# Performance work log

Hardware: AMD Instinct MI355X
Metric: run time of the kernel (lower is better)

Reference implementation:

```python
import jax, jax.numpy as jnp
import numpy as np

EPS = 1e-7  # keras.backend.epsilon()


def setup_inputs() -> dict:
    key = jax.random.key(0)
    k1, k2, k3 = jax.random.split(key, 3)
    B, N, D_in, C, D_out = 32, 2048, 8, 32, 16
    x = jax.random.normal(k1, (B, N, D_in), dtype=jnp.float32)
    W = jax.random.normal(k2, (1, N, C, D_out, D_in), dtype=jnp.float32) * 0.05
    R = jax.random.normal(k3, (1, N, C), dtype=jnp.float32)
    return {"x": x, "W": W, "R": R}


def reference(x, W, R):
    # x: [B, N, D_in]; W: [1, N, C, D_out, D_in]; R: [1, N, C]
    R_nor = jax.nn.softmax(R[0], axis=0)          # softmax over N (axis=1 of [1,N,C])
    # per-capsule transform: u[b,n,c,j] = sum_k W[n,c,j,k] * x[b,n,k]
    u = jnp.einsum('ncjk,bnk->bncj', W[0], x)
    # routing-weighted aggregation over input capsules n
    s = jnp.einsum('bncj,nc->bcj', u, R_nor)      # [B, C, D_out]
    # squash along capsule dim (original axis=-2 before squeeze == D_out)
    ss = jnp.sum(jnp.square(s), axis=-1, keepdims=True) + EPS
    scale = jnp.sqrt(ss) / (1.0 + ss)
    return scale * s                               # [B, C, D_out]
```

## Files before the change

kernel.cpp:

```cpp
#include <hip/hip_runtime.h>
#include <math.h>


#define NN 2048
#define CC 32

__device__ __forceinline__ void g2l16(const float* g, float* l) {
  __builtin_amdgcn_global_load_lds((const __attribute__((address_space(1))) void*)g,
                                   (__attribute__((address_space(3))) void*)l, 16, 0, 0);
}

__global__ void caps_stats(const float* __restrict__ R, float* __restrict__ I) {
  const int c = blockIdx.x;
  const int t = threadIdx.x;
  __shared__ float red[256];
  float s = 0.f;
#pragma unroll
  for (int i = 0; i < 8; ++i) s += expf(R[(size_t)(t + i * 256) * CC + c]);
  red[t] = s;
  __syncthreads();
  for (int h = 128; h >= 1; h >>= 1) {
    if (t < h) red[t] += red[t + h];
    __syncthreads();
  }
  if (t == 0) I[c] = 1.0f / red[0];
}

__global__ void __launch_bounds__(512) caps_main(const float* __restrict__ x,
                                                 const float* __restrict__ W,
                                                 const float* __restrict__ R,
                                                 const float* __restrict__ I,
                                                 float* __restrict__ P) {
  const int bid = blockIdx.x;
  const int cg = bid >> 6;
  const int chunk = bid & 63;
  const int n0 = chunk * 32;
  const int tid = threadIdx.x;
  const int ws = tid >> 6;
  const int lane = tid & 63;
  const int j = lane & 15;
  const int bo = lane >> 4;

  extern __shared__ float smem[];
  float* wREG = smem + ws * 4096;
  float* wW = wREG;
  float* wX = wREG + 3072;
  const int nw = n0 + ws * 4;

  float4 iv0 = *(const float4*)(I + cg * 8);
  float4 iv1 = *(const float4*)(I + cg * 8 + 4);
  float4 rq0[4], rq1[4];
#pragma unroll
  for (int nl = 0; nl < 4; ++nl) {
    rq0[nl] = *(const float4*)(R + (size_t)(nw + nl) * CC + cg * 8);
    rq1[nl] = *(const float4*)(R + (size_t)(nw + nl) * CC + cg * 8 + 4);
  }

  auto stageW = [&](int nl, int buf) {
#pragma unroll
    for (int i = 0; i < 4; ++i) {
      int S = i * 64 + lane;
      int g = S ^ ((S >> 3) & 3);
      g2l16(W + (size_t)(nw + nl) * 4096 + cg * 1024 + g * 4,
            wW + buf * 1024 + i * 256);
    }
  };

  stageW(0, 0);
  {
    int g2 = lane ^ ((lane >> 4) << 1);
    int b = g2 >> 1, kq = g2 & 1;
    const float* xs = x + (size_t)b * (NN * 8) + kq * 4;
#pragma unroll
    for (int nl = 0; nl < 4; ++nl)
      g2l16(xs + (size_t)(nw + nl) * 8, wX + nl * 256);
  }
  stageW(1, 1);

  float rv[4][8];
#pragma unroll
  for (int nl = 0; nl < 4; ++nl) {
    rv[nl][0] = expf(rq0[nl].x) * iv0.x;
    rv[nl][1] = expf(rq0[nl].y) * iv0.y;
    rv[nl][2] = expf(rq0[nl].z) * iv0.z;
    rv[nl][3] = expf(rq0[nl].w) * iv0.w;
    rv[nl][4] = expf(rq1[nl].x) * iv1.x;
    rv[nl][5] = expf(rq1[nl].y) * iv1.y;
    rv[nl][6] = expf(rq1[nl].z) * iv1.z;
    rv[nl][7] = expf(rq1[nl].w) * iv1.w;
  }

  float acc[8][8];
#pragma unroll
  for (int a = 0; a < 8; ++a)
#pragma unroll
    for (int b = 0; b < 8; ++b) acc[a][b] = 0.f;

  auto compute = [&](int nl, int buf) {
    const float* Wn = wW + buf * 1024;
    const float* Xn = wX + nl * 256;
#pragma unroll
    for (int kh = 0; kh < 2; ++kh) {
      float4 xv[8];
#pragma unroll
      for (int bi = 0; bi < 8; ++bi) {
        int G = (bo * 8 + bi) * 2 + kh;
        int S = G ^ ((G >> 4) << 1);
        xv[bi] = *(const float4*)(Xn + S * 4);
      }
#pragma unroll
      for (int ci = 0; ci < 8; ++ci) {
        int slot = (ci * 32 + j * 2 + kh) ^ (j >> 2);
        float4 wf = *(const float4*)(Wn + slot * 4);
        float rvv = rv[nl][ci];
        float w0 = wf.x * rvv, w1 = wf.y * rvv, w2 = wf.z * rvv, w3 = wf.w * rvv;
#pragma unroll
        for (int bi = 0; bi < 8; ++bi) {
          float a = acc[ci][bi];
          a = fmaf(w0, xv[bi].x, a);
          a = fmaf(w1, xv[bi].y, a);
          a = fmaf(w2, xv[bi].z, a);
          a = fmaf(w3, xv[bi].w, a);
          acc[ci][bi] = a;
        }
      }
    }
  };

  stageW(2, 2);
  asm volatile("s_waitcnt vmcnt(8)" ::: "memory");
  __builtin_amdgcn_sched_barrier(0);
  compute(0, 0);
  asm volatile("s_waitcnt lgkmcnt(0)" ::: "memory");
  __builtin_amdgcn_sched_barrier(0);
  stageW(3, 0);
  asm volatile("s_waitcnt vmcnt(8)" ::: "memory");
  __builtin_amdgcn_sched_barrier(0);
  compute(1, 1);
  asm volatile("s_waitcnt vmcnt(4)" ::: "memory");
  __builtin_amdgcn_sched_barrier(0);
  compute(2, 2);
  asm volatile("s_waitcnt vmcnt(0)" ::: "memory");
  __builtin_amdgcn_sched_barrier(0);
  compute(3, 0);

#pragma unroll
  for (int ci = 0; ci < 8; ++ci)
#pragma unroll
    for (int bi = 0; bi < 8; ++bi)
      wREG[(ci * 8 + bi) * 64 + lane] = acc[ci][bi];
  __syncthreads();
  {
    float ssum[8];
#pragma unroll
    for (int i = 0; i < 8; ++i) ssum[i] = 0.f;
#pragma unroll
    for (int w = 0; w < 8; ++w)
#pragma unroll
      for (int i = 0; i < 8; ++i)
        ssum[i] += smem[(size_t)w * 4096 + (ws * 8 + i) * 64 + lane];
#pragma unroll
    for (int i = 0; i < 8; ++i)
      P[(size_t)bid * 4096 + (ws * 8 + i) * 64 + lane] = ssum[i];
  }
}

__global__ void caps_reduce(const float* __restrict__ P, float* __restrict__ out) {
  const int g = blockIdx.x * 256 + threadIdx.x;
  const int j = g & 15;
  const int c = (g >> 4) & 31;
  const int b = g >> 9;
  const int bo = b >> 3, bi = b & 7;
  const int cg = c >> 3, ci = c & 7;
  const int idx = (ci * 8 + bi) * 64 + (bo * 16 + j);
  const float* Pq = P + (size_t)cg * 64 * 4096 + idx;

  float s = 0.f;
#pragma unroll 16
  for (int ch = 0; ch < 64; ++ch) {
    s += Pq[(size_t)ch * 4096];
  }
  float sq = s * s;
  sq += __shfl_xor(sq, 8, 16);
  sq += __shfl_xor(sq, 4, 16);
  sq += __shfl_xor(sq, 2, 16);
  sq += __shfl_xor(sq, 1, 16);
  float ss = sq + 1e-7f;
  float scale = sqrtf(ss) / (1.0f + ss);
  out[g] = scale * s;
}

extern "C" void kernel_launch(void* const* d_in, const int* in_sizes, int n_in,
                              void* d_out, int out_size, void* d_ws, size_t ws_size,
                              hipStream_t stream) {
  const float* x = (const float*)d_in[0];
  const float* W = (const float*)d_in[1];
  const float* R = (const float*)d_in[2];
  float* out = (float*)d_out;

  float* I = (float*)d_ws;
  float* P = (float*)d_ws + 64;

  hipFuncSetAttribute((const void*)caps_main,
                      hipFuncAttributeMaxDynamicSharedMemorySize, 131072);

  caps_stats<<<32, 256, 0, stream>>>(R, I);
  caps_main<<<256, 512, 131072, stream>>>(x, W, R, I, P);
  caps_reduce<<<64, 256, 0, stream>>>(P, out);
}
```

Baseline: 28.68 us.

## Fold softmax normalization into reduce kernel and double main-kernel grid

Removes the separate softmax-statistics kernel. The main kernel now uses unnormalized exp(R) weights, and the reduce kernel computes the per-capsule denominator and applies it after summing partials. The main kernel's grid doubles to 512 blocks, each covering 16 input capsules, with less LDS per block and a two-phase cross-wave reduction. The goal is one fewer launch and better occupancy and parallelism. The cost is twice as many partials to reduce and each reduce block redundantly recomputing the exp sums over R.

```diff
diff --git a/kernel.cpp b/kernel.cpp
--- a/kernel.cpp
+++ b/kernel.cpp
@@ -10,31 +10,14 @@
                                    (__attribute__((address_space(3))) void*)l, 16, 0, 0);
 }
 
-__global__ void caps_stats(const float* __restrict__ R, float* __restrict__ I) {
-  const int c = blockIdx.x;
-  const int t = threadIdx.x;
-  __shared__ float red[256];
-  float s = 0.f;
-#pragma unroll
-  for (int i = 0; i < 8; ++i) s += expf(R[(size_t)(t + i * 256) * CC + c]);
-  red[t] = s;
-  __syncthreads();
-  for (int h = 128; h >= 1; h >>= 1) {
-    if (t < h) red[t] += red[t + h];
-    __syncthreads();
-  }
-  if (t == 0) I[c] = 1.0f / red[0];
-}
-
 __global__ void __launch_bounds__(512) caps_main(const float* __restrict__ x,
                                                  const float* __restrict__ W,
                                                  const float* __restrict__ R,
-                                                 const float* __restrict__ I,
                                                  float* __restrict__ P) {
   const int bid = blockIdx.x;
-  const int cg = bid >> 6;
-  const int chunk = bid & 63;
-  const int n0 = chunk * 32;
+  const int cg = bid >> 7;
+  const int chunk = bid & 127;
+  const int n0 = chunk * 16;
   const int tid = threadIdx.x;
   const int ws = tid >> 6;
   const int lane = tid & 63;
@@ -42,19 +25,15 @@
   const int bo = lane >> 4;
 
   extern __shared__ float smem[];
-  float* wREG = smem + ws * 4096;
+  float* wREG = smem + ws * 2560;
   float* wW = wREG;
-  float* wX = wREG + 3072;
-  const int nw = n0 + ws * 4;
+  float* wX = wREG + 2048;
+  const int nw = n0 + ws * 2;
 
-  float4 iv0 = *(const float4*)(I + cg * 8);
-  float4 iv1 = *(const float4*)(I + cg * 8 + 4);
-  float4 rq0[4], rq1[4];
-#pragma unroll
-  for (int nl = 0; nl < 4; ++nl) {
-    rq0[nl] = *(const float4*)(R + (size_t)(nw + nl) * CC + cg * 8);
-    rq1[nl] = *(const float4*)(R + (size_t)(nw + nl) * CC + cg * 8 + 4);
-  }
+  float4 ra0 = *(const float4*)(R + (size_t)nw * CC + cg * 8);
+  float4 ra1 = *(const float4*)(R + (size_t)nw * CC + cg * 8 + 4);
+  float4 rb0 = *(const float4*)(R + (size_t)(nw + 1) * CC + cg * 8);
+  float4 rb1 = *(const float4*)(R + (size_t)(nw + 1) * CC + cg * 8 + 4);
 
   auto stageW = [&](int nl, int buf) {
 #pragma unroll
@@ -71,24 +50,16 @@
     int g2 = lane ^ ((lane >> 4) << 1);
     int b = g2 >> 1, kq = g2 & 1;
     const float* xs = x + (size_t)b * (NN * 8) + kq * 4;
-#pragma unroll
-    for (int nl = 0; nl < 4; ++nl)
-      g2l16(xs + (size_t)(nw + nl) * 8, wX + nl * 256);
+    g2l16(xs + (size_t)nw * 8, wX);
+    g2l16(xs + (size_t)(nw + 1) * 8, wX + 256);
   }
   stageW(1, 1);
 
-  float rv[4][8];
-#pragma unroll
-  for (int nl = 0; nl < 4; ++nl) {
-    rv[nl][0] = expf(rq0[nl].x) * iv0.x;
-    rv[nl][1] = expf(rq0[nl].y) * iv0.y;
-    rv[nl][2] = expf(rq0[nl].z) * iv0.z;
-    rv[nl][3] = expf(rq0[nl].w) * iv0.w;
-    rv[nl][4] = expf(rq1[nl].x) * iv1.x;
-    rv[nl][5] = expf(rq1[nl].y) * iv1.y;
-    rv[nl][6] = expf(rq1[nl].z) * iv1.z;
-    rv[nl][7] = expf(rq1[nl].w) * iv1.w;
-  }
+  float rv[2][8];
+  rv[0][0] = expf(ra0.x); rv[0][1] = expf(ra0.y); rv[0][2] = expf(ra0.z); rv[0][3] = expf(ra0.w);
+  rv[0][4] = expf(ra1.x); rv[0][5] = expf(ra1.y); rv[0][6] = expf(ra1.z); rv[0][7] = expf(ra1.w);
+  rv[1][0] = expf(rb0.x); rv[1][1] = expf(rb0.y); rv[1][2] = expf(rb0.z); rv[1][3] = expf(rb0.w);
+  rv[1][4] = expf(rb1.x); rv[1][5] = expf(rb1.y); rv[1][6] = expf(rb1.z); rv[1][7] = expf(rb1.w);
 
   float acc[8][8];
 #pragma unroll
@@ -127,59 +98,75 @@
     }
   };
 
-  stageW(2, 2);
-  asm volatile("s_waitcnt vmcnt(8)" ::: "memory");
+  asm volatile("s_waitcnt vmcnt(4)" ::: "memory");
   __builtin_amdgcn_sched_barrier(0);
   compute(0, 0);
-  asm volatile("s_waitcnt lgkmcnt(0)" ::: "memory");
-  __builtin_amdgcn_sched_barrier(0);
-  stageW(3, 0);
-  asm volatile("s_waitcnt vmcnt(8)" ::: "memory");
+  asm volatile("s_waitcnt vmcnt(0)" ::: "memory");
   __builtin_amdgcn_sched_barrier(0);
   compute(1, 1);
-  asm volatile("s_waitcnt vmcnt(4)" ::: "memory");
-  __builtin_amdgcn_sched_barrier(0);
-  compute(2, 2);
-  asm volatile("s_waitcnt vmcnt(0)" ::: "memory");
-  __builtin_amdgcn_sched_barrier(0);
-  compute(3, 0);
 
 #pragma unroll
-  for (int ci = 0; ci < 8; ++ci)
+  for (int phase = 0; phase < 2; ++phase) {
 #pragma unroll
-    for (int bi = 0; bi < 8; ++bi)
-      wREG[(ci * 8 + bi) * 64 + lane] = acc[ci][bi];
-  __syncthreads();
-  {
-    float ssum[8];
+    for (int cl = 0; cl < 4; ++cl)
 #pragma unroll
-    for (int i = 0; i < 8; ++i) ssum[i] = 0.f;
+      for (int bi = 0; bi < 8; ++bi)
+        wREG[(cl * 8 + bi) * 64 + lane] = acc[phase * 4 + cl][bi];
+    __syncthreads();
+    {
+      float ssum[4] = {0.f, 0.f, 0.f, 0.f};
 #pragma unroll
-    for (int w = 0; w < 8; ++w)
+      for (int w = 0; w < 8; ++w)
 #pragma unroll
-      for (int i = 0; i < 8; ++i)
-        ssum[i] += smem[(size_t)w * 4096 + (ws * 8 + i) * 64 + lane];
+        for (int i = 0; i < 4; ++i)
+          ssum[i] += smem[(size_t)w * 2560 + (ws * 4 + i) * 64 + lane];
 #pragma unroll
-    for (int i = 0; i < 8; ++i)
-      P[(size_t)bid * 4096 + (ws * 8 + i) * 64 + lane] = ssum[i];
+      for (int i = 0; i < 4; ++i)
+        P[(size_t)bid * 4096 + (phase * 32 + ws * 4 + i) * 64 + lane] = ssum[i];
+    }
+    __syncthreads();
   }
 }
 
-__global__ void caps_reduce(const float* __restrict__ P, float* __restrict__ out) {
-  const int g = blockIdx.x * 256 + threadIdx.x;
+__global__ void caps_reduce(const float* __restrict__ P, const float* __restrict__ R,
+                            float* __restrict__ out) {
+  const int t = threadIdx.x;
+  const int bid = blockIdx.x;
+  const int g = bid * 128 + t;
   const int j = g & 15;
   const int c = (g >> 4) & 31;
   const int b = g >> 9;
   const int bo = b >> 3, bi = b & 7;
   const int cg = c >> 3, ci = c & 7;
+
+  __shared__ float red[128];
+  __shared__ float invd[8];
+  {
+    const int cl = t & 7, nt = t >> 3;
+    const int c0 = (bid * 8) & 31;
+    float s = 0.f;
+#pragma unroll 8
+    for (int i = 0; i < 128; ++i)
+      s += expf(R[(size_t)(nt + i * 16) * CC + c0 + cl]);
+    red[t] = s;
+  }
+  __syncthreads();
+#pragma unroll
+  for (int h = 8; h >= 1; h >>= 1) {
+    if ((t >> 3) < h) red[t] += red[t + h * 8];
+    __syncthreads();
+  }
+  if (t < 8) invd[t] = 1.0f / red[t];
+  __syncthreads();
+
   const int idx = (ci * 8 + bi) * 64 + (bo * 16 + j);
-  const float* Pq = P + (size_t)cg * 64 * 4096 + idx;
-
+  const float* Pq = P + (size_t)cg * 128 * 4096 + idx;
   float s = 0.f;
 #pragma unroll 16
-  for (int ch = 0; ch < 64; ++ch) {
+  for (int ch = 0; ch < 128; ++ch)
     s += Pq[(size_t)ch * 4096];
-  }
+  s *= invd[c & 7];
+
   float sq = s * s;
   sq += __shfl_xor(sq, 8, 16);
   sq += __shfl_xor(sq, 4, 16);
@@ -197,14 +184,11 @@
   const float* W = (const float*)d_in[1];
   const float* R = (const float*)d_in[2];
   float* out = (float*)d_out;
-
-  float* I = (float*)d_ws;
-  float* P = (float*)d_ws + 64;
+  float* P = (float*)d_ws;
 
   hipFuncSetAttribute((const void*)caps_main,
-                      hipFuncAttributeMaxDynamicSharedMemorySize, 131072);
+                      hipFuncAttributeMaxDynamicSharedMemorySize, 81920);
 
-  caps_stats<<<32, 256, 0, stream>>>(R, I);
-  caps_main<<<256, 512, 131072, stream>>>(x, W, R, I, P);
-  caps_reduce<<<64, 256, 0, stream>>>(P, out);
+  caps_main<<<512, 512, 81920, stream>>>(x, W, R, P);
+  caps_reduce<<<128, 128, 0, stream>>>(P, R, out);
 }
```

After: 38.31 us. 33.6% more time.
